# Kernel tuning notes

Measured on AMD Instinct MI355X. Metric: run time of the kernel, lower is better.

The kernel has to match this reference:

```python
import jax, jax.numpy as jnp
import numpy as np

EPS = 1e-5
N, E, G = 65536, 262144, 256
DV, DE, DG = 256, 128, 256


def _ln(x):
    # LayerNorm without affine over the last dim
    mu = jnp.mean(x, axis=-1, keepdims=True)
    var = jnp.mean(jnp.square(x - mu), axis=-1, keepdims=True)
    return (x - mu) * jax.lax.rsqrt(var + EPS)


def setup_inputs() -> dict:
    key = jax.random.key(0)
    ks = jax.random.split(key, 14)
    inp = {
        'fv': jax.random.normal(ks[0], (N, DV), jnp.float32),
        'fe': jax.random.normal(ks[1], (E, DE), jnp.float32),
        'fg': jax.random.normal(ks[2], (G, DG), jnp.float32),
        'fv_pos': jax.random.normal(ks[3], (N, 3), jnp.float32),
        'fv_c': jax.random.normal(ks[4], (N, DV), jnp.float32),
        'fe_c': jax.random.normal(ks[5], (E, DE), jnp.float32),
        'fv_pos_c': jax.random.normal(ks[6], (N, DV), jnp.float32),
        # learned params (original zero-inits the modulation Linears; we use
        # small random weights so the kernel path is exercised)
        'W_v': jax.random.normal(ks[7], (2 * DV, DV), jnp.float32) * 0.02,
        'b_v': jnp.zeros((2 * DV,), jnp.float32),
        'W_vpos': jax.random.normal(ks[8], (DE, DV), jnp.float32) * 0.02,
        'b_vpos': jnp.zeros((DE,), jnp.float32),
        'W_e': jax.random.normal(ks[9], (2 * DE, DE), jnp.float32) * 0.02,
        'b_e': jnp.zeros((2 * DE,), jnp.float32),
        'g_gamma': jnp.ones((DG,), jnp.float32),
        'g_beta': jnp.zeros((DG,), jnp.float32),
        'W_pos': jax.random.normal(ks[10], (1, DG), jnp.float32) * 0.02,
        'b_pos': jnp.zeros((1,), jnp.float32),
        'src': jax.random.randint(ks[11], (E,), 0, N, jnp.int32),
        'dst': jax.random.randint(ks[12], (E,), 0, N, jnp.int32),
        'node_gid': (jnp.arange(N, dtype=jnp.int32) // (N // G)),
    }
    return inp


def reference(fv, fe, fg, fv_pos, fv_c, fe_c, fv_pos_c,
              W_v, b_v, W_vpos, b_vpos, W_e, b_e,
              g_gamma, g_beta, W_pos, b_pos,
              src, dst, node_gid):
    act = jax.nn.silu
    # --- node modulation ---
    mod_v = act(fv_c + fv_pos_c) @ W_v.T + b_v            # [N, 2*DV]
    shift_v, scale_v = jnp.split(mod_v, 2, axis=1)
    fv_out = _ln(fv) * (1.0 + scale_v) + shift_v
    # --- edge modulation with gsddmm('add') gather ---
    fvp = fv_pos_c @ W_vpos.T + b_vpos                    # [N, DE]
    fv2e = fvp[src] + fvp[dst]                            # sddmm add [E, DE]
    mod_e = act(fe_c + fv2e) @ W_e.T + b_e                # [E, 2*DE]
    shift_e, scale_e = jnp.split(mod_e, 2, axis=1)
    fe_out = _ln(fe) * (1.0 + scale_e) + shift_e
    # --- adaptive position scale-norm (per-graph, equivariant) ---
    ones = jnp.ones((N,), fv_pos.dtype)
    cnt = jax.ops.segment_sum(ones, node_gid, num_segments=G)          # [G]
    mean = jax.ops.segment_sum(fv_pos, node_gid, num_segments=G) / cnt[:, None]
    centered = fv_pos - mean[node_gid]                                  # [N, 3]
    sq = jax.ops.segment_sum(jnp.sum(jnp.square(centered), axis=1), node_gid, num_segments=G)
    rms = jnp.sqrt(sq / (cnt * 3.0) + EPS)                              # [G]
    pos_n = centered / rms[node_gid][:, None]
    s = act(fg) @ W_pos.T + b_pos                                       # [G, 1]
    fv_pos_out = pos_n * (1.0 + s)[node_gid]
    # --- graph LayerNorm (affine) ---
    fg_out = _ln(fg) * g_gamma + g_beta
    return (fv_out, fe_out, fg_out, fv_pos_out)
```

## Files before the change

### kernel.cpp

```cpp
#include <hip/hip_runtime.h>

#define N_NODES 65536
#define N_EDGES 262144
#define N_GRAPH 256
#define DV 256
#define DE 128
#define DG 256
#define EPS 1e-5f

typedef __bf16 bf16_t;
typedef bf16_t bf16x8 __attribute__((ext_vector_type(8)));
typedef float f32x4 __attribute__((ext_vector_type(4)));
typedef unsigned short ushort_t;

__device__ __forceinline__ float silu_f(float x) {
  return x / (1.0f + __expf(-x));
}
__device__ __forceinline__ unsigned short f2bf(float f) {
  unsigned int u = __float_as_uint(f);
  u += 0x7fffu + ((u >> 16) & 1u);
  return (unsigned short)(u >> 16);
}
__device__ __forceinline__ float bf2f(unsigned short h) {
  return __uint_as_float(((unsigned int)h) << 16);
}
__device__ __forceinline__ void split_bf(float x, ushort_t& hi, ushort_t& lo) {
  hi = f2bf(x);
  lo = f2bf(x - bf2f(hi));
}
__device__ __forceinline__ void wave_reduce2(float& s1, float& s2) {
  #pragma unroll
  for (int off = 32; off > 0; off >>= 1) {
    s1 += __shfl_xor(s1, off);
    s2 += __shfl_xor(s2, off);
  }
}

__global__ __launch_bounds__(256) void k_prep(
    const float* __restrict__ W_v, const float* __restrict__ W_e,
    const float* __restrict__ W_vpos, ushort_t* __restrict__ Wv_bf,
    ushort_t* __restrict__ We_bf, ushort_t* __restrict__ Wvpos_bf) {
  int idx = blockIdx.x * 256 + threadIdx.x;
  const float* s;
  ushort_t* d;
  int o;
  if (idx < 32768) { s = W_v; d = Wv_bf; o = idx; }
  else if (idx < 40960) { s = W_e; d = We_bf; o = idx - 32768; }
  else { s = W_vpos; d = Wvpos_bf; o = idx - 40960; }
  float4 v = *(const float4*)&s[(size_t)o * 4];
  ushort4 r;
  r.x = f2bf(v.x); r.y = f2bf(v.y); r.z = f2bf(v.z); r.w = f2bf(v.w);
  *(ushort4*)&d[(size_t)o * 4] = r;
}

__global__ __launch_bounds__(512) void k_fvp(
    const float* __restrict__ fv_pos_c, const ushort_t* __restrict__ Wvpos_bf,
    const float* __restrict__ b_vpos, ushort_t* __restrict__ fvp_bf) {
  __shared__ __align__(16) ushort_t Xh[32][264];
  __shared__ __align__(16) ushort_t Xl[32][264];
  const int tid = threadIdx.x;
  const int l = tid & 63, w = tid >> 6;
  const int m0 = blockIdx.x * 32;
  #pragma unroll
  for (int i = 0; i < 4; ++i) {
    int idx = i * 512 + tid;
    int r = idx >> 6, c4 = idx & 63;
    float4 v = *(const float4*)&fv_pos_c[(size_t)(m0 + r) * DV + c4 * 4];
    ushort4 h, lo;
    split_bf(v.x, h.x, lo.x);
    split_bf(v.y, h.y, lo.y);
    split_bf(v.z, h.z, lo.z);
    split_bf(v.w, h.w, lo.w);
    *(ushort4*)&Xh[r][c4 * 4] = h;
    *(ushort4*)&Xl[r][c4 * 4] = lo;
  }
  __syncthreads();
  f32x4 acc[2];
  acc[0] = (f32x4)(0.f);
  acc[1] = (f32x4)(0.f);
  const int mrow = (w & 1) * 16;
  const int ncol0 = (w >> 1) * 32;
  const int arow = mrow + (l & 15);
  for (int kc = 0; kc < 8; ++kc) {
    int ke = kc * 32 + (l >> 4) * 8;
    bf16x8 ah = *(const bf16x8*)&Xh[arow][ke];
    bf16x8 al = *(const bf16x8*)&Xl[arow][ke];
    #pragma unroll
    for (int ni = 0; ni < 2; ++ni) {
      bf16x8 b = *(const bf16x8*)&Wvpos_bf[(size_t)(ncol0 + ni * 16 + (l & 15)) * DV + ke];
      acc[ni] = __builtin_amdgcn_mfma_f32_16x16x32_bf16(al, b, acc[ni], 0, 0, 0);
      acc[ni] = __builtin_amdgcn_mfma_f32_16x16x32_bf16(ah, b, acc[ni], 0, 0, 0);
    }
  }
  #pragma unroll
  for (int ni = 0; ni < 2; ++ni) {
    int col = ncol0 + ni * 16 + (l & 15);
    float bias = b_vpos[col];
    #pragma unroll
    for (int j = 0; j < 4; ++j) {
      int row = m0 + mrow + (l >> 4) * 4 + j;
      fvp_bf[(size_t)row * DE + col] = f2bf(acc[ni][j] + bias);
    }
  }
}

__global__ __launch_bounds__(512) void k_node(
    const float* __restrict__ fv, const float* __restrict__ fv_c,
    const float* __restrict__ fv_pos_c, const ushort_t* __restrict__ Wv_bf,
    const float* __restrict__ b_v, float* __restrict__ fv_out) {
  __shared__ __align__(16) ushort_t Xh[32][264];
  __shared__ __align__(16) ushort_t Xl[32][264];
  __shared__ float muL[32], rsL[32];
  const int tid = threadIdx.x;
  const int l = tid & 63, w = tid >> 6;
  const int m0 = blockIdx.x * 32;
  #pragma unroll
  for (int i = 0; i < 4; ++i) {
    int idx = i * 512 + tid;
    int r = idx >> 6, c4 = idx & 63;
    size_t g = (size_t)(m0 + r) * DV + c4 * 4;
    float4 a = *(const float4*)&fv_c[g];
    float4 b = *(const float4*)&fv_pos_c[g];
    ushort4 h, lo;
    split_bf(silu_f(a.x + b.x), h.x, lo.x);
    split_bf(silu_f(a.y + b.y), h.y, lo.y);
    split_bf(silu_f(a.z + b.z), h.z, lo.z);
    split_bf(silu_f(a.w + b.w), h.w, lo.w);
    *(ushort4*)&Xh[r][c4 * 4] = h;
    *(ushort4*)&Xl[r][c4 * 4] = lo;
  }
  #pragma unroll
  for (int rr = 0; rr < 4; ++rr) {
    int row = w * 4 + rr;
    float4 v = *(const float4*)&fv[(size_t)(m0 + row) * DV + l * 4];
    float s1 = v.x + v.y + v.z + v.w;
    float s2 = v.x * v.x + v.y * v.y + v.z * v.z + v.w * v.w;
    wave_reduce2(s1, s2);
    if (l == 0) {
      float mu = s1 * (1.0f / DV);
      float var = s2 * (1.0f / DV) - mu * mu;
      muL[row] = mu;
      rsL[row] = rsqrtf(var + EPS);
    }
  }
  __syncthreads();
  f32x4 acc[2][4];
  #pragma unroll
  for (int mi = 0; mi < 2; ++mi)
    #pragma unroll
    for (int ni = 0; ni < 4; ++ni) acc[mi][ni] = (f32x4)(0.f);
  int ncol[4];
  ncol[0] = w * 32;
  ncol[1] = w * 32 + 16;
  ncol[2] = DV + w * 32;
  ncol[3] = DV + w * 32 + 16;
  for (int kc = 0; kc < 8; ++kc) {
    int ke = kc * 32 + (l >> 4) * 8;
    bf16x8 ah[2], al[2];
    #pragma unroll
    for (int mi = 0; mi < 2; ++mi) {
      ah[mi] = *(const bf16x8*)&Xh[mi * 16 + (l & 15)][ke];
      al[mi] = *(const bf16x8*)&Xl[mi * 16 + (l & 15)][ke];
    }
    #pragma unroll
    for (int ni = 0; ni < 4; ++ni) {
      bf16x8 b = *(const bf16x8*)&Wv_bf[(size_t)(ncol[ni] + (l & 15)) * DV + ke];
      #pragma unroll
      for (int mi = 0; mi < 2; ++mi) {
        acc[mi][ni] = __builtin_amdgcn_mfma_f32_16x16x32_bf16(al[mi], b, acc[mi][ni], 0, 0, 0);
        acc[mi][ni] = __builtin_amdgcn_mfma_f32_16x16x32_bf16(ah[mi], b, acc[mi][ni], 0, 0, 0);
      }
    }
  }
  #pragma unroll
  for (int ni2 = 0; ni2 < 2; ++ni2) {
    int c = w * 32 + ni2 * 16 + (l & 15);
    float bsh = b_v[c];
    float bsc = b_v[DV + c];
    #pragma unroll
    for (int mi = 0; mi < 2; ++mi)
      #pragma unroll
      for (int j = 0; j < 4; ++j) {
        int row = mi * 16 + (l >> 4) * 4 + j;
        size_t g = (size_t)(m0 + row) * DV + c;
        float v = fv[g];
        float sh = acc[mi][ni2][j] + bsh;
        float sc = acc[mi][ni2 + 2][j] + bsc;
        fv_out[g] = (v - muL[row]) * rsL[row] * (1.0f + sc) + sh;
      }
  }
}

__global__ __launch_bounds__(512) void k_edge(
    const float* __restrict__ fe, const float* __restrict__ fe_c,
    const ushort_t* __restrict__ fvp_bf, const int* __restrict__ src,
    const int* __restrict__ dst, const ushort_t* __restrict__ We_bf,
    const float* __restrict__ b_e, float* __restrict__ fe_out) {
  __shared__ __align__(16) ushort_t Xh[64][136];
  __shared__ __align__(16) ushort_t Xl[64][136];
  __shared__ float muL[64], rsL[64];
  const int tid = threadIdx.x;
  const int l = tid & 63, w = tid >> 6;
  const int m0 = blockIdx.x * 64;
  #pragma unroll
  for (int i = 0; i < 4; ++i) {
    int idx = i * 512 + tid;
    int r = idx >> 5, c4 = idx & 31;
    int sr = src[m0 + r], dr = dst[m0 + r];
    float4 a = *(const float4*)&fe_c[(size_t)(m0 + r) * DE + c4 * 4];
    ushort4 p = *(const ushort4*)&fvp_bf[(size_t)sr * DE + c4 * 4];
    ushort4 q = *(const ushort4*)&fvp_bf[(size_t)dr * DE + c4 * 4];
    ushort4 h, lo;
    split_bf(silu_f(a.x + bf2f(p.x) + bf2f(q.x)), h.x, lo.x);
    split_bf(silu_f(a.y + bf2f(p.y) + bf2f(q.y)), h.y, lo.y);
    split_bf(silu_f(a.z + bf2f(p.z) + bf2f(q.z)), h.z, lo.z);
    split_bf(silu_f(a.w + bf2f(p.w) + bf2f(q.w)), h.w, lo.w);
    *(ushort4*)&Xh[r][c4 * 4] = h;
    *(ushort4*)&Xl[r][c4 * 4] = lo;
  }
  #pragma unroll
  for (int rr = 0; rr < 8; ++rr) {
    int row = w * 8 + rr;
    float2 v = *(const float2*)&fe[(size_t)(m0 + row) * DE + l * 2];
    float s1 = v.x + v.y;
    float s2 = v.x * v.x + v.y * v.y;
    wave_reduce2(s1, s2);
    if (l == 0) {
      float mu = s1 * (1.0f / DE);
      float var = s2 * (1.0f / DE) - mu * mu;
      muL[row] = mu;
      rsL[row] = rsqrtf(var + EPS);
    }
  }
  __syncthreads();
  f32x4 acc[4][2];
  #pragma unroll
  for (int mi = 0; mi < 4; ++mi) {
    acc[mi][0] = (f32x4)(0.f);
    acc[mi][1] = (f32x4)(0.f);
  }
  for (int kc = 0; kc < 4; ++kc) {
    int ke = kc * 32 + (l >> 4) * 8;
    bf16x8 ah[4], al[4];
    #pragma unroll
    for (int mi = 0; mi < 4; ++mi) {
      ah[mi] = *(const bf16x8*)&Xh[mi * 16 + (l & 15)][ke];
      al[mi] = *(const bf16x8*)&Xl[mi * 16 + (l & 15)][ke];
    }
    #pragma unroll
    for (int ni = 0; ni < 2; ++ni) {
      bf16x8 b = *(const bf16x8*)&We_bf[(size_t)(ni * DE + w * 16 + (l & 15)) * DE + ke];
      #pragma unroll
      for (int mi = 0; mi < 4; ++mi) {
        acc[mi][ni] = __builtin_amdgcn_mfma_f32_16x16x32_bf16(al[mi], b, acc[mi][ni], 0, 0, 0);
        acc[mi][ni] = __builtin_amdgcn_mfma_f32_16x16x32_bf16(ah[mi], b, acc[mi][ni], 0, 0, 0);
      }
    }
  }
  {
    int c = w * 16 + (l & 15);
    float bsh = b_e[c];
    float bsc = b_e[DE + c];
    #pragma unroll
    for (int mi = 0; mi < 4; ++mi)
      #pragma unroll
      for (int j = 0; j < 4; ++j) {
        int row = mi * 16 + (l >> 4) * 4 + j;
        size_t g = (size_t)(m0 + row) * DE + c;
        float v = fe[g];
        float sh = acc[mi][0][j] + bsh;
        float sc = acc[mi][1][j] + bsc;
        fe_out[g] = (v - muL[row]) * rsL[row] * (1.0f + sc) + sh;
      }
  }
}

__global__ __launch_bounds__(256) void k_fg_pos(
    const float* __restrict__ fg, const float* __restrict__ g_gamma,
    const float* __restrict__ g_beta, const float* __restrict__ W_pos,
    const float* __restrict__ b_pos, const float* __restrict__ fv_pos,
    const int* __restrict__ node_gid, float* __restrict__ fg_out,
    float* __restrict__ pos_out) {
  const int g = blockIdx.x, t = threadIdx.x;
  const int lane = t & 63, wave = t >> 6;
  __shared__ float p1[4], p2[4], p3[4];
  __shared__ float px[4], py[4], pz[4], pq[4];
  float x = fg[g * DG + t];
  float sv = silu_f(x) * W_pos[t];
  float s1 = x, s2 = x * x, s3 = sv;
  #pragma unroll
  for (int off = 32; off > 0; off >>= 1) {
    s1 += __shfl_xor(s1, off);
    s2 += __shfl_xor(s2, off);
    s3 += __shfl_xor(s3, off);
  }
  if (lane == 0) { p1[wave] = s1; p2[wave] = s2; p3[wave] = s3; }
  __syncthreads();
  s1 = p1[0] + p1[1] + p1[2] + p1[3];
  s2 = p2[0] + p2[1] + p2[2] + p2[3];
  float mu = s1 * (1.0f / DG);
  float var = s2 * (1.0f / DG) - mu * mu;
  float rstd = rsqrtf(var + EPS);
  fg_out[g * DG + t] = (x - mu) * rstd * g_gamma[t] + g_beta[t];
  float s_own = (p3[0] + p3[1] + p3[2] + p3[3]) + b_pos[0];
  const int i = g * 256 + t;
  const int gid = node_gid[i];
  float vx = fv_pos[3 * i + 0];
  float vy = fv_pos[3 * i + 1];
  float vz = fv_pos[3 * i + 2];
  if (__syncthreads_and(gid == g)) {
    float rx = vx, ry = vy, rz = vz, rq = vx * vx + vy * vy + vz * vz;
    #pragma unroll
    for (int off = 32; off > 0; off >>= 1) {
      rx += __shfl_xor(rx, off);
      ry += __shfl_xor(ry, off);
      rz += __shfl_xor(rz, off);
      rq += __shfl_xor(rq, off);
    }
    if (lane == 0) { px[wave] = rx; py[wave] = ry; pz[wave] = rz; pq[wave] = rq; }
    __syncthreads();
    float sx = px[0] + px[1] + px[2] + px[3];
    float sy = py[0] + py[1] + py[2] + py[3];
    float sz = pz[0] + pz[1] + pz[2] + pz[3];
    float sq = pq[0] + pq[1] + pq[2] + pq[3];
    float ic = 1.0f / 256.0f;
    float mx = sx * ic, my = sy * ic, mz = sz * ic;
    float cq = fmaxf(sq - 256.0f * (mx * mx + my * my + mz * mz), 0.0f);
    float rms = sqrtf(cq / (256.0f * 3.0f) + EPS);
    float sc = (1.0f + s_own) / rms;
    pos_out[3 * i + 0] = (vx - mx) * sc;
    pos_out[3 * i + 1] = (vy - my) * sc;
    pos_out[3 * i + 2] = (vz - mz) * sc;
  } else {
    float sx = 0.f, sy = 0.f, sz = 0.f, sq = 0.f, cnt = 0.f;
    for (int j = 0; j < N_NODES; ++j) {
      if (node_gid[j] == gid) {
        float ax = fv_pos[3 * j + 0];
        float ay = fv_pos[3 * j + 1];
        float az = fv_pos[3 * j + 2];
        sx += ax; sy += ay; sz += az;
        sq += ax * ax + ay * ay + az * az;
        cnt += 1.0f;
      }
    }
    float ic = 1.0f / fmaxf(cnt, 1.0f);
    float mx = sx * ic, my = sy * ic, mz = sz * ic;
    float cq = fmaxf(sq - cnt * (mx * mx + my * my + mz * mz), 0.0f);
    float rms = sqrtf(cq / (cnt * 3.0f) + EPS);
    float sg = 0.f;
    for (int c = 0; c < DG; ++c) sg += silu_f(fg[gid * DG + c]) * W_pos[c];
    float sc = (1.0f + sg + b_pos[0]) / rms;
    pos_out[3 * i + 0] = (vx - mx) * sc;
    pos_out[3 * i + 1] = (vy - my) * sc;
    pos_out[3 * i + 2] = (vz - mz) * sc;
  }
}

extern "C" void kernel_launch(void* const* d_in, const int* in_sizes, int n_in,
                              void* d_out, int out_size, void* d_ws,
                              size_t ws_size, hipStream_t stream) {
  const float* fv = (const float*)d_in[0];
  const float* fe = (const float*)d_in[1];
  const float* fg = (const float*)d_in[2];
  const float* fv_pos = (const float*)d_in[3];
  const float* fv_c = (const float*)d_in[4];
  const float* fe_c = (const float*)d_in[5];
  const float* fv_pos_c = (const float*)d_in[6];
  const float* W_v = (const float*)d_in[7];
  const float* b_v = (const float*)d_in[8];
  const float* W_vpos = (const float*)d_in[9];
  const float* b_vpos = (const float*)d_in[10];
  const float* W_e = (const float*)d_in[11];
  const float* b_e = (const float*)d_in[12];
  const float* g_gamma = (const float*)d_in[13];
  const float* g_beta = (const float*)d_in[14];
  const float* W_pos = (const float*)d_in[15];
  const float* b_pos = (const float*)d_in[16];
  const int* src = (const int*)d_in[17];
  const int* dst = (const int*)d_in[18];
  const int* node_gid = (const int*)d_in[19];

  float* out = (float*)d_out;
  float* fv_out = out;
  float* fe_out = fv_out + (size_t)N_NODES * DV;
  float* fg_out = fe_out + (size_t)N_EDGES * DE;
  float* pos_out = fg_out + (size_t)N_GRAPH * DG;

  char* ws = (char*)d_ws;
  ushort_t* fvp_bf = (ushort_t*)ws;
  ushort_t* Wv_bf = (ushort_t*)(ws + 16777216);
  ushort_t* We_bf = (ushort_t*)(ws + 16777216 + 262144);
  ushort_t* Wvpos_bf = (ushort_t*)(ws + 16777216 + 262144 + 65536);

  k_prep<<<192, 256, 0, stream>>>(W_v, W_e, W_vpos, Wv_bf, We_bf, Wvpos_bf);
  k_fvp<<<N_NODES / 32, 512, 0, stream>>>(fv_pos_c, Wvpos_bf, b_vpos, fvp_bf);
  k_node<<<N_NODES / 32, 512, 0, stream>>>(fv, fv_c, fv_pos_c, Wv_bf, b_v, fv_out);
  k_edge<<<N_EDGES / 64, 512, 0, stream>>>(fe, fe_c, fvp_bf, src, dst, We_bf,
                                           b_e, fe_out);
  k_fg_pos<<<N_GRAPH, 256, 0, stream>>>(fg, g_gamma, g_beta, W_pos, b_pos,
                                        fv_pos, node_gid, fg_out, pos_out);
}
```

Before: 301.7 us.

## Restructure edge kernel to per-wave 16-edge tiles held in registers

The edge kernel now assigns 16 edges per wave, builds the silu(fe_c + gathered fvp) A-operand directly in registers as bf16 hi/lo pairs, and computes all 256 output columns per wave, with no shared memory and no block barrier. LayerNorm statistics come from 16-lane shuffles over fe values already loaded in the MFMA output layout. The block size drops to 256, and f2bf now uses the native bf16 conversion. The aim is to remove LDS staging and synchronisation, at the cost of every wave reloading the full W_e from cache and higher register pressure from 16 accumulators.

```diff
diff --git a/kernel.cpp b/kernel.cpp
--- a/kernel.cpp
+++ b/kernel.cpp
@@ -16,12 +16,11 @@
 __device__ __forceinline__ float silu_f(float x) {
   return x / (1.0f + __expf(-x));
 }
-__device__ __forceinline__ unsigned short f2bf(float f) {
-  unsigned int u = __float_as_uint(f);
-  u += 0x7fffu + ((u >> 16) & 1u);
-  return (unsigned short)(u >> 16);
-}
-__device__ __forceinline__ float bf2f(unsigned short h) {
+__device__ __forceinline__ ushort_t f2bf(float f) {
+  bf16_t h = (bf16_t)f;
+  return __builtin_bit_cast(ushort_t, h);
+}
+__device__ __forceinline__ float bf2f(ushort_t h) {
   return __uint_as_float(((unsigned int)h) << 16);
 }
 __device__ __forceinline__ void split_bf(float x, ushort_t& hi, ushort_t& lo) {
@@ -191,88 +190,91 @@
   }
 }
 
-__global__ __launch_bounds__(512) void k_edge(
+__global__ __launch_bounds__(256) void k_edge(
     const float* __restrict__ fe, const float* __restrict__ fe_c,
     const ushort_t* __restrict__ fvp_bf, const int* __restrict__ src,
     const int* __restrict__ dst, const ushort_t* __restrict__ We_bf,
     const float* __restrict__ b_e, float* __restrict__ fe_out) {
-  __shared__ __align__(16) ushort_t Xh[64][136];
-  __shared__ __align__(16) ushort_t Xl[64][136];
-  __shared__ float muL[64], rsL[64];
   const int tid = threadIdx.x;
-  const int l = tid & 63, w = tid >> 6;
-  const int m0 = blockIdx.x * 64;
-  #pragma unroll
-  for (int i = 0; i < 4; ++i) {
-    int idx = i * 512 + tid;
-    int r = idx >> 5, c4 = idx & 31;
-    int sr = src[m0 + r], dr = dst[m0 + r];
-    float4 a = *(const float4*)&fe_c[(size_t)(m0 + r) * DE + c4 * 4];
-    ushort4 p = *(const ushort4*)&fvp_bf[(size_t)sr * DE + c4 * 4];
-    ushort4 q = *(const ushort4*)&fvp_bf[(size_t)dr * DE + c4 * 4];
-    ushort4 h, lo;
-    split_bf(silu_f(a.x + bf2f(p.x) + bf2f(q.x)), h.x, lo.x);
-    split_bf(silu_f(a.y + bf2f(p.y) + bf2f(q.y)), h.y, lo.y);
-    split_bf(silu_f(a.z + bf2f(p.z) + bf2f(q.z)), h.z, lo.z);
-    split_bf(silu_f(a.w + bf2f(p.w) + bf2f(q.w)), h.w, lo.w);
-    *(ushort4*)&Xh[r][c4 * 4] = h;
-    *(ushort4*)&Xl[r][c4 * 4] = lo;
-  }
-  #pragma unroll
-  for (int rr = 0; rr < 8; ++rr) {
-    int row = w * 8 + rr;
-    float2 v = *(const float2*)&fe[(size_t)(m0 + row) * DE + l * 2];
-    float s1 = v.x + v.y;
-    float s2 = v.x * v.x + v.y * v.y;
-    wave_reduce2(s1, s2);
-    if (l == 0) {
-      float mu = s1 * (1.0f / DE);
-      float var = s2 * (1.0f / DE) - mu * mu;
-      muL[row] = mu;
-      rsL[row] = rsqrtf(var + EPS);
-    }
-  }
-  __syncthreads();
-  f32x4 acc[4][2];
-  #pragma unroll
-  for (int mi = 0; mi < 4; ++mi) {
-    acc[mi][0] = (f32x4)(0.f);
-    acc[mi][1] = (f32x4)(0.f);
-  }
+  const int l = tid & 63;
+  const int wid = blockIdx.x * 4 + (tid >> 6);
+  const int e0 = wid * 16;
+  const int sub = l & 15, quad = l >> 4;
+  const int erow = e0 + sub;
+  const int sr = src[erow], dr = dst[erow];
+  bf16x8 ah[4], al[4];
+  const float* fcb = fe_c + (size_t)erow * DE + quad * 8;
+  const ushort_t* pb = fvp_bf + (size_t)sr * DE + quad * 8;
+  const ushort_t* qb = fvp_bf + (size_t)dr * DE + quad * 8;
+  #pragma unroll
   for (int kc = 0; kc < 4; ++kc) {
-    int ke = kc * 32 + (l >> 4) * 8;
-    bf16x8 ah[4], al[4];
-    #pragma unroll
-    for (int mi = 0; mi < 4; ++mi) {
-      ah[mi] = *(const bf16x8*)&Xh[mi * 16 + (l & 15)][ke];
-      al[mi] = *(const bf16x8*)&Xl[mi * 16 + (l & 15)][ke];
-    }
-    #pragma unroll
-    for (int ni = 0; ni < 2; ++ni) {
-      bf16x8 b = *(const bf16x8*)&We_bf[(size_t)(ni * DE + w * 16 + (l & 15)) * DE + ke];
-      #pragma unroll
-      for (int mi = 0; mi < 4; ++mi) {
-        acc[mi][ni] = __builtin_amdgcn_mfma_f32_16x16x32_bf16(al[mi], b, acc[mi][ni], 0, 0, 0);
-        acc[mi][ni] = __builtin_amdgcn_mfma_f32_16x16x32_bf16(ah[mi], b, acc[mi][ni], 0, 0, 0);
-      }
-    }
-  }
-  {
-    int c = w * 16 + (l & 15);
-    float bsh = b_e[c];
-    float bsc = b_e[DE + c];
-    #pragma unroll
-    for (int mi = 0; mi < 4; ++mi)
-      #pragma unroll
-      for (int j = 0; j < 4; ++j) {
-        int row = mi * 16 + (l >> 4) * 4 + j;
-        size_t g = (size_t)(m0 + row) * DE + c;
-        float v = fe[g];
-        float sh = acc[mi][0][j] + bsh;
-        float sc = acc[mi][1][j] + bsc;
-        fe_out[g] = (v - muL[row]) * rsL[row] * (1.0f + sc) + sh;
-      }
-  }
+    float4 f0 = *(const float4*)(fcb + kc * 32);
+    float4 f1 = *(const float4*)(fcb + kc * 32 + 4);
+    bf16x8 p = *(const bf16x8*)(pb + kc * 32);
+    bf16x8 q = *(const bf16x8*)(qb + kc * 32);
+    float xv[8] = {f0.x, f0.y, f0.z, f0.w, f1.x, f1.y, f1.z, f1.w};
+    #pragma unroll
+    for (int j = 0; j < 8; ++j) {
+      float x = silu_f(xv[j] + (float)p[j] + (float)q[j]);
+      bf16_t h = (bf16_t)x;
+      ah[kc][j] = h;
+      al[kc][j] = (bf16_t)(x - (float)h);
+    }
+  }
+  f32x4 acc[16];
+  #pragma unroll
+  for (int ni = 0; ni < 16; ++ni) acc[ni] = (f32x4)(0.f);
+  const ushort_t* wb = We_bf + (size_t)sub * DE + quad * 8;
+  #pragma unroll
+  for (int kc = 0; kc < 4; ++kc) {
+    #pragma unroll
+    for (int ni = 0; ni < 16; ++ni) {
+      bf16x8 b = *(const bf16x8*)(wb + (size_t)ni * 16 * DE + kc * 32);
+      acc[ni] = __builtin_amdgcn_mfma_f32_16x16x32_bf16(al[kc], b, acc[ni], 0, 0, 0);
+      acc[ni] = __builtin_amdgcn_mfma_f32_16x16x32_bf16(ah[kc], b, acc[ni], 0, 0, 0);
+    }
+  }
+  float fev[4][8];
+  #pragma unroll
+  for (int j = 0; j < 4; ++j)
+    #pragma unroll
+    for (int ci = 0; ci < 8; ++ci)
+      fev[j][ci] = fe[(size_t)(e0 + quad * 4 + j) * DE + ci * 16 + sub];
+  float mu[4], rs[4];
+  #pragma unroll
+  for (int j = 0; j < 4; ++j) {
+    float s1 = 0.f, s2 = 0.f;
+    #pragma unroll
+    for (int ci = 0; ci < 8; ++ci) {
+      float v = fev[j][ci];
+      s1 += v;
+      s2 += v * v;
+    }
+    #pragma unroll
+    for (int off = 1; off < 16; off <<= 1) {
+      s1 += __shfl_xor(s1, off);
+      s2 += __shfl_xor(s2, off);
+    }
+    float m = s1 * (1.0f / DE);
+    float var = s2 * (1.0f / DE) - m * m;
+    mu[j] = m;
+    rs[j] = rsqrtf(var + EPS);
+  }
+  float bsh[8], bsc[8];
+  #pragma unroll
+  for (int ci = 0; ci < 8; ++ci) {
+    bsh[ci] = b_e[ci * 16 + sub];
+    bsc[ci] = b_e[DE + ci * 16 + sub];
+  }
+  #pragma unroll
+  for (int j = 0; j < 4; ++j)
+    #pragma unroll
+    for (int ci = 0; ci < 8; ++ci) {
+      float sh = acc[ci][j] + bsh[ci];
+      float sc = acc[ci + 8][j] + bsc[ci];
+      size_t g = (size_t)(e0 + quad * 4 + j) * DE + ci * 16 + sub;
+      fe_out[g] = (fev[j][ci] - mu[j]) * rs[j] * (1.0f + sc) + sh;
+    }
 }
 
 __global__ __launch_bounds__(256) void k_fg_pos(
@@ -395,7 +397,7 @@
   k_prep<<<192, 256, 0, stream>>>(W_v, W_e, W_vpos, Wv_bf, We_bf, Wvpos_bf);
   k_fvp<<<N_NODES / 32, 512, 0, stream>>>(fv_pos_c, Wvpos_bf, b_vpos, fvp_bf);
   k_node<<<N_NODES / 32, 512, 0, stream>>>(fv, fv_c, fv_pos_c, Wv_bf, b_v, fv_out);
-  k_edge<<<N_EDGES / 64, 512, 0, stream>>>(fe, fe_c, fvp_bf, src, dst, We_bf,
+  k_edge<<<N_EDGES / 64, 256, 0, stream>>>(fe, fe_c, fvp_bf, src, dst, We_bf,
                                            b_e, fe_out);
   k_fg_pos<<<N_GRAPH, 256, 0, stream>>>(fg, g_gamma, g_beta, W_pos, b_pos,
                                         fv_pos, node_gid, fg_out, pos_out);
```

Result: slower. 373.4 us (+23.8%).
